# Optimization experiments

Hardware: AMD Instinct MI355X
Metric: run time of the kernel (lower is better)

Reference implementation:

```python
import jax, jax.numpy as jnp
import numpy as np

EMBED = 128; HEADS = 4; NUM_CLASSES = 20; NUM_LAYERS = 2
SCENE = (128, 128, 16)
NQ = SCENE[0] * SCENE[1] * SCENE[2]
NI = 300
IMG = (96, 320); ORI = (384, 1280)
VOXEL_SIZE = 0.2
SCORE_THR, MASK_THR, IOU_THR = 0.25, 0.5, 0.8


def _image_grid():
    # generate_grid(image_shape, ori_image_shape), then flip(dims=[0]) -> (x, y) pixel coords in ori resolution
    ys = jnp.arange(IMG[0], dtype=jnp.float32) * (ORI[0] / IMG[0])
    xs = jnp.arange(IMG[1], dtype=jnp.float32) * (ORI[1] / IMG[1])
    gy, gx = jnp.meshgrid(ys, xs, indexing='ij')
    return jnp.stack([gx, gy], 0)  # (2, h, w)


def _scene_pos():
    g = jnp.stack(jnp.meshgrid(*[jnp.arange(s, dtype=jnp.float32) for s in SCENE], indexing='ij'), 0)
    g = (g + 0.5) * VOXEL_SIZE  # project_scale = 1
    return g.reshape(3, -1).T  # (NQ, 3)


def _layernorm(x, g, b):
    mu = x.mean(-1, keepdims=True)
    var = ((x - mu) ** 2).mean(-1, keepdims=True)
    return (x - mu) * jax.lax.rsqrt(var + 1e-5) * g + b


def _mha(q, k, v, w, b):
    # w: (4, D, D) = Wq, Wk, Wv, Wo; b: (4, D)
    B, Nq, D = q.shape; hd = D // HEADS
    def proj(x, i):
        return (x @ w[i].T + b[i]).reshape(B, -1, HEADS, hd).transpose(0, 2, 1, 3)
    qh, kh, vh = proj(q, 0), proj(k, 1), proj(v, 2)
    attn = jax.nn.softmax(jnp.einsum('bhqd,bhkd->bhqk', qh, kh) / jnp.sqrt(jnp.float32(hd)), axis=-1)
    o = jnp.einsum('bhqk,bhkd->bhqd', attn, vh).transpose(0, 2, 1, 3).reshape(B, Nq, D)
    return o @ w[3].T + b[3]


def _tlayer(q, k, v, aw, ab, lg, lb, w1, b1, w2, b2):
    x = _layernorm(q + _mha(q, k, v, aw, ab), lg[0], lb[0])
    h = jax.nn.relu(x @ w1.T + b1) @ w2.T + b2
    return _layernorm(x + h, lg[1], lb[1])


def setup_inputs():
    key = jax.random.key(0)
    ks = jax.random.split(key, 20)
    h, w = IMG
    queries = jax.random.normal(ks[0], (1, NI, EMBED), jnp.float32)
    # 8 instances get a strong class logit so exactly they pass score_thr
    pred_logits = 0.1 * jax.random.normal(ks[1], (1, NI, NUM_CLASSES + 1), jnp.float32)
    ii = jnp.arange(8)
    pred_logits = pred_logits.at[0, ii, ii % (NUM_CLASSES + 1)].add(6.0)
    # each kept instance owns a disjoint 40-px-wide strip -> passes IoU>=0.8
    pred_masks = -6.0 + 0.1 * jax.random.normal(ks[2], (1, NI, h, w), jnp.float32)
    strip = jnp.arange(w) // 40  # 0..7
    boost = 12.0 * (jnp.arange(NI)[:, None] == strip[None, :]).astype(jnp.float32)
    pred_masks = pred_masks + boost[None, :, None, :]
    x3d = 0.1 * jax.random.normal(ks[3], (1, EMBED) + SCENE, jnp.float32)
    depth = 1.0 + 49.0 * jax.random.uniform(ks[4], (1, h, w), jnp.float32)
    K = jnp.array([[[500.0, 0.0, 160.0], [0.0, 500.0, 48.0], [0.0, 0.0, 1.0]]], jnp.float32)
    E = jnp.array([[[1.0, 0.0, 0.0, 0.5], [0.0, 1.0, 0.0, 1.0], [0.0, 0.0, 1.0, 1.5], [0.0, 0.0, 0.0, 1.0]]], jnp.float32)
    voxel_origin = jnp.array([[[0.0, -12.8, -2.0]]], jnp.float32)
    fov_mask = jax.random.bernoulli(ks[5], 0.25, (1, NQ))
    L = NUM_LAYERS
    scene_embed_w = 0.02 * jax.random.normal(ks[6], (NQ, EMBED), jnp.float32)
    inst_pos_w = 0.02 * jax.random.normal(ks[7], (NI, EMBED), jnp.float32)
    pos_w = 0.02 * jax.random.normal(ks[8], (EMBED, 3), jnp.float32)
    conv_w = 0.05 * jax.random.normal(ks[9], (NUM_CLASSES, EMBED), jnp.float32)
    conv_b = jnp.zeros((NUM_CLASSES,), jnp.float32)
    attn_w = 0.05 * jax.random.normal(ks[10], (L, 2, 4, EMBED, EMBED), jnp.float32)
    attn_b = jnp.zeros((L, 2, 4, EMBED), jnp.float32)
    ln_g = jnp.ones((L, 2, 2, EMBED), jnp.float32)
    ln_b = jnp.zeros((L, 2, 2, EMBED), jnp.float32)
    ffn_w1 = 0.05 * jax.random.normal(ks[11], (L, 2, 4 * EMBED, EMBED), jnp.float32)
    ffn_b1 = jnp.zeros((L, 2, 4 * EMBED), jnp.float32)
    ffn_w2 = 0.05 * jax.random.normal(ks[12], (L, 2, EMBED, 4 * EMBED), jnp.float32)
    ffn_b2 = jnp.zeros((L, 2, EMBED), jnp.float32)
    return dict(queries=queries, pred_logits=pred_logits, pred_masks=pred_masks, x3d=x3d, depth=depth,
                K=K, E=E, voxel_origin=voxel_origin, fov_mask=fov_mask,
                scene_embed_w=scene_embed_w, inst_pos_w=inst_pos_w, pos_w=pos_w, conv_w=conv_w, conv_b=conv_b,
                attn_w=attn_w, attn_b=attn_b, ln_g=ln_g, ln_b=ln_b,
                ffn_w1=ffn_w1, ffn_b1=ffn_b1, ffn_w2=ffn_w2, ffn_b2=ffn_b2)


def reference(queries, pred_logits, pred_masks, x3d, depth, K, E, voxel_origin, fov_mask,
              scene_embed_w, inst_pos_w, pos_w, conv_w, conv_b,
              attn_w, attn_b, ln_g, ln_b, ffn_w1, ffn_b1, ffn_w2, ffn_b2):
    h, w = IMG
    # ---- panoptic_postprocess (bs == 1) ----
    sig = jax.nn.sigmoid(pred_logits[0])
    prob_cls = jax.nn.softmax(sig / 0.06, axis=-1)
    scores = prob_cls.max(-1); labels = prob_cls.argmax(-1)
    keep = (labels != prob_cls.shape[-1]) & (scores > SCORE_THR)
    kidx = jnp.nonzero(keep)[0]
    pm = jax.nn.sigmoid(pred_masks[0])[kidx]          # (k, h, w)
    sk = scores[kidx]
    mids = (sk[:, None, None] * pm).argmax(0)          # per-pixel winning instance
    masks = mids[None] == jnp.arange(pm.shape[0])[:, None, None]
    marea = masks.reshape(pm.shape[0], -1).sum(1)
    pmb = pm >= MASK_THR
    parea = pmb.reshape(pm.shape[0], -1).sum(1)
    masks = masks & pmb
    keep_ = (masks.reshape(pm.shape[0], -1).sum(1) > 0) & (marea / parea >= IOU_THR)
    sel = jnp.nonzero(keep_)[0]
    inst_masks = masks[sel]                             # (k2, h, w)
    k2idx = kidx[sel]                                   # final kept slots in [0, NI)
    # ---- gather_mask_pos (depth already at (h, w) -> interpolate is identity) ----
    ig = _image_grid()
    ig3 = jnp.concatenate([ig[None] * depth[:, None], depth[:, None]], axis=1)  # (1,3,h,w) = (x*d, y*d, d)
    cam = jnp.linalg.inv(K) @ ig3.reshape(1, 3, -1)
    homo = jnp.concatenate([cam, jnp.ones((1, 1, h * w), cam.dtype)], axis=1)
    world = (jnp.linalg.inv(E) @ homo)[0, :3].T        # (hw, 3)
    xyz = inst_masks.reshape(inst_masks.shape[0], -1).astype(world.dtype) @ world  # masked sum per instance
    mask_pos = xyz @ pos_w.T                            # Linear(3, embed, bias=False)
    inst_q = queries[0][k2idx][None]                    # (1, k2, D)
    inst_p = (inst_pos_w[k2idx] + mask_pos)[None]
    # ---- scene tokens ----
    scene_embed_full = scene_embed_w[None] + x3d.reshape(1, EMBED, NQ).transpose(0, 2, 1)
    qsrc = scene_embed_full
    fidx = jnp.nonzero(fov_mask[0])[0]
    se = scene_embed_full[:, fidx]
    sp = ((_scene_pos()[None] + voxel_origin)[:, fidx]) @ pos_w.T
    for i in range(NUM_LAYERS):
        inst_q = _tlayer(inst_q + inst_p, se + sp, se, attn_w[i, 0], attn_b[i, 0], ln_g[i, 0], ln_b[i, 0],
                         ffn_w1[i, 0], ffn_b1[i, 0], ffn_w2[i, 0], ffn_b2[i, 0])
        se = _tlayer(se + sp, inst_q + inst_p, inst_q, attn_w[i, 1], attn_b[i, 1], ln_g[i, 1], ln_b[i, 1],
                     ffn_w1[i, 1], ffn_b1[i, 1], ffn_w2[i, 1], ffn_b2[i, 1])
    # ---- index_fov_back_to_voxels + cls_head (project_scale==1 -> Identity + 1x1 Conv3d) ----
    full = qsrc.at[:, fidx].set(se)
    x3d_ = full.transpose(0, 2, 1).reshape(1, EMBED, *SCENE)
    out = jnp.einsum('bcxyz,oc->boxyz', x3d_, conv_w) + conv_b.reshape(1, -1, 1, 1, 1)
    return out
```

## Files before the change

kernel.cpp:

```cpp
#include <hip/hip_runtime.h>
#include <math.h>

#define EMBED 128
#define NCLS 21
#define NI_ 300
#define IMH 96
#define IMW 320
#define NPIX (IMH*IMW)
#define NQ 262144
#define NF_MAX 73728
#define INST_MAX 16
#define IH_MAX 64
#define RS32 0.17677669529663687f

#define S_NF 0
#define S_NK 1
#define S_NINST 2
#define S_NIH 3
#define S_INVK 8
#define S_INVE 24
#define S_KIDX 64
#define S_SKK 400
#define S_MAREA 768
#define S_PAREA 1088
// ... 173 lines not shown
  int base=blockIdx.x*1024;
  int s=0;
  for (int k=0;k<4;k++) s += (fov[base+k*256+t]!=0)?1:0;
  red[t]=s; __syncthreads();
  for (int st=128;st>0;st>>=1){ if(t<st) red[t]+=red[t+st]; __syncthreads(); }
  if (t==0) iw[S_FCNT+blockIdx.x]=red[0];
}

__global__ void k_fov_scan(float* ws){
  int* iw=(int*)ws;
  if (threadIdx.x==0){
    int acc=0;
    for (int b=0;b<256;b++){ iw[S_FOFF+b]=acc; acc+=iw[S_FCNT+b]; }
    iw[S_NF]=(acc<NF_MAX)?acc:NF_MAX;
  }
}

__global__ __launch_bounds__(256) void k_fov_scatter(const int* fov, float* ws){
  int* iw=(int*)ws;
  int* fidx=(int*)((char*)ws+OFF_FIDX);
  int* invr=(int*)((char*)ws+OFF_INV);
  __shared__ int wsums[4];
  __shared__ int woff[4];
  __shared__ int cur;
  __shared__ int tot;
  int t=threadIdx.x; int w=t>>6; int lane=t&63;
  if (t==0) cur=iw[S_FOFF+blockIdx.x];
  __syncthreads();
  int base=blockIdx.x*1024;
  for (int k=0;k<4;k++){
    int i=base+k*256+t;
    int f=(fov[i]!=0)?1:0;
    unsigned long long m=__ballot(f);
    int rk=__popcll(m & ((lane==0)?0ull:((~0ull)>>(64-lane))));
    if (lane==0) wsums[w]=__popcll(m);
    __syncthreads();
    if (t==0){ int a=0; for(int q2=0;q2<4;q2++){ woff[q2]=a; a+=wsums[q2]; } tot=a; }
    __syncthreads();
    if (f){
      int r=cur+woff[w]+rk;
      if (r<NF_MAX){ fidx[r]=i; invr[i]=r; } else invr[i]=-1;
    } else invr[i]=-1;
    __syncthreads();
    if (t==0) cur+=tot;
    __syncthreads();
  }
}

__global__ __launch_bounds__(256) void k_se_build(const float* sew, const float* x3d, const int* fidx, float* SE, float* ws){
  int* iw=(int*)ws;
  int nf=iw[S_NF];
  int r0=blockIdx.x*64;
  if (r0>=nf) return;
  int nr=min(64,nf-r0);
  __shared__ float tile[64][129];
  __shared__ int fidxl[64];
  int t=threadIdx.x;
  if (t<64) fidxl[t]=(t<nr)? fidx[r0+t]:0;
  __syncthreads();
  for (int idx=t; idx<64*128; idx+=256){
    int v=idx>>7, e=idx&127;
    tile[v][e]=(v<nr)? sew[(size_t)fidxl[v]*128+e]:0.f;
  }
  __syncthreads();
  for (int idx=t; idx<128*64; idx+=256){
    int c=idx>>6, v=idx&63;
    if (v<nr) tile[v][c]+=x3d[(size_t)c*NQ+fidxl[v]];
  }
  __syncthreads();
  for (int idx=t; idx<64*128; idx+=256){
    int v=idx>>7, e=idx&127;
    if (v<nr) SE[(r0+v)*128+e]=tile[v][e];
  }
}

__global__ __launch_bounds__(256) void kA_prep(const float* Wq, const float* bq, const float* Wk, const float* bk, float* ws){
  int* iw=(int*)ws; float* fw=ws;
  int n=iw[S_NINST]; int nih=iw[S_NIH];
  int t=threadIdx.x;
  for (int idx=t; idx<n*128; idx+=256) fw[S_QIN+idx]=fw[S_INSTQ+idx]+fw[S_INSTP+idx];
  __syncthreads();
  for (int idx=t; idx<n*128; idx+=256){
    int i=idx>>7, e=idx&127;
    float a=bq[e];
    for (int k=0;k<128;k++) a+=fw[S_QIN+i*128+k]*Wq[e*128+k];
    fw[S_QH+idx]=a;
  }
  __syncthreads();
  for (int idx=t; idx<nih*128; idx+=256){
    int ih=idx>>7, e=idx&127;
    int i=ih>>2, h=ih&3;
    float a=0.f;
    for (int d=0;d<32;d++) a+=fw[S_QH+i*128+h*32+d]*Wk[(h*32+d)*128+e];
    fw[S_QKT+idx]=a*RS32;
  }
  for (int ih=t; ih<nih; ih+=256){
    int i=ih>>2, h=ih&3;
    float a=0.f;
    for (int d=0;d<32;d++) a+=fw[S_QH+i*128+h*32+d]*bk[h*32+d];
    fw[S_SB+ih]=a*RS32;
  }
}

__global__ __launch_bounds__(256) void kS1(const float* SE, float* SC, const float* posw, const float* org, const int* fidx, float* ws){
  int* iw=(int*)ws; float* fw=ws;
  int nf=iw[S_NF]; int nih=iw[S_NIH];
  int r0=blockIdx.x*64;
  if (r0>=nf || nih==0) return;
  int nr=min(64,nf-r0);
  __shared__ float xt[64][129];
  __shared__ float qk[IH_MAX*128];
  __shared__ float sbl[IH_MAX];
  __shared__ float pwl[384];
  __shared__ float px[64],py[64],pz[64];
  __shared__ int fidxl[64];
  int t=threadIdx.x;
  for (int i=t;i<384;i+=256) pwl[i]=posw[i];
  if (t<64) fidxl[t]=(t<nr)? fidx[r0+t]:0;
  for (int idx=t; idx<nih*128; idx+=256) qk[idx]=fw[S_QKT+idx];
  if (t<IH_MAX) sbl[t]=(t<nih)? fw[S_SB+t]:0.f;
  __syncthreads();
  if (t<64){
    int q=fidxl[t];
    int vx=q>>11, vy=(q>>4)&127, vz=q&15;
    px[t]=(vx+0.5f)*0.2f+org[0];
    py[t]=(vy+0.5f)*0.2f+org[1];
    pz[t]=(vz+0.5f)*0.2f+org[2];
  }
  __syncthreads();
  for (int idx=t; idx<64*128; idx+=256){
    int v=idx>>7, e=idx&127;
    float val=0.f;
    if (v<nr) val=SE[(r0+v)*128+e]+px[v]*pwl[e*3]+py[v]*pwl[e*3+1]+pz[v]*pwl[e*3+2];
    xt[v][e]=val;
  }
  __syncthreads();
  int tokl=t&63, base=t>>6;
  for (int ih=base; ih<nih; ih+=4){
    float a=sbl[ih];
    const float* qrow=qk+ih*128;
    for (int e=0;e<128;e++) a+=qrow[e]*xt[tokl][e];
    if (tokl<nr) SC[(size_t)ih*NF_MAX+r0+tokl]=a;
  }
}

__global__ __launch_bounds__(256) void kS2S3(float* SC, float* ws){
  int* iw=(int*)ws; float* fw=ws;
  int nih=iw[S_NIH]; int ih=blockIdx.x;
  if (ih>=nih) return;
  int nf=iw[S_NF];
  float* row=SC+(size_t)ih*NF_MAX;
  __shared__ float red[256];
  int t=threadIdx.x;
  float m=-1e30f;
  for (int j=t;j<nf;j+=256) m=fmaxf(m,row[j]);
  red[t]=m; __syncthreads();
  for (int s=128;s>0;s>>=1){ if(t<s) red[t]=fmaxf(red[t],red[t+s]); __syncthreads(); }
  m=red[0]; __syncthreads();
  float sum=0.f;
  for (int j=t;j<nf;j+=256){ float p=expf(row[j]-m); row[j]=p; sum+=p; }
  red[t]=sum; __syncthreads();
  for (int s=128;s>0;s>>=1){ if(t<s) red[t]+=red[t+s]; __syncthreads(); }
  if (t==0) fw[S_SUMV+ih]=red[0];
  if (t<128) fw[S_WSUM+ih*128+t]=0.f;
}

__global__ __launch_bounds__(256) void kS4(const float* SC, const float* SE, float* ws){
  int* iw=(int*)ws; float* fw=ws;
  int nf=iw[S_NF]; int nih=iw[S_NIH];
  if (nih==0) return;
  int t=threadIdx.x;
  int chunk=(nf+255)/256;
  int j0=blockIdx.x*chunk;
  int j1=min(nf,j0+chunk);
  if (j0>=j1) return;
  __shared__ float pt[64*64];
  int e=t&127, half=t>>7;
  float acc[32];
  #pragma unroll
  for (int r=0;r<32;r++) acc[r]=0.f;
  for (int jj=j0; jj<j1; jj+=64){
    int cnt=min(64,j1-jj);
    __syncthreads();
    for (int idx=t; idx<64*64; idx+=256){
      int ih=idx>>6, jl=idx&63;
      pt[idx]=(ih<nih && jl<cnt)? SC[(size_t)ih*NF_MAX+jj+jl]:0.f;
    }
    __syncthreads();
    for (int jl=0; jl<cnt; jl++){
      float sv=SE[(jj+jl)*128+e];
      #pragma unroll
      for (int r=0;r<32;r++) acc[r]+=pt[(half*32+r)*64+jl]*sv;
    }
  }
  #pragma unroll
  for (int r=0;r<32;r++) atomicAdd(&fw[S_WSUM+(half*32+r)*128+e], acc[r]);
}

__global__ __launch_bounds__(256) void kA_post(const float* Wv, const float* bv, const float* Wo, const float* bo,
    const float* g, const float* bb, float* ws){
  int* iw=(int*)ws; float* fw=ws;
  int n=iw[S_NINST]; int nih=iw[S_NIH];
  __shared__ float wn[IH_MAX*128];
  __shared__ float ol[INST_MAX*128];
  __shared__ float tl[INST_MAX*128];
  int t=threadIdx.x;
  for (int idx=t; idx<nih*128; idx+=256){
    int ih=idx>>7;
    wn[idx]=fw[S_WSUM+idx]/fw[S_SUMV+ih];
  }
  __syncthreads();
  for (int idx=t; idx<n*128; idx+=256){
    int i=idx>>7, f=idx&127; int h=f>>5;
    float a=bv[f];
    const float* wrow=Wv+f*128;
    const float* wv=wn+(i*4+h)*128;
    for (int e2=0;e2<128;e2++) a+=wrow[e2]*wv[e2];
    ol[idx]=a;
  }
  __syncthreads();
  for (int idx=t; idx<n*128; idx+=256){
    int i=idx>>7, e2=idx&127;
    float a=bo[e2];
    const float* orow=ol+i*128;
    const float* wrow=Wo+e2*128;
    for (int f2=0;f2<128;f2++) a+=orow[f2]*wrow[f2];
    tl[idx]=a+fw[S_QIN+idx];
  }
  __syncthreads();
  int w=t>>6, lane=t&63;
  for (int i=w;i<n;i+=4){
    float v0=tl[i*128+lane], v1=tl[i*128+64+lane];
    float s=v0+v1;
    for (int o=32;o>0;o>>=1) s+=__shfl_xor(s,o);
    float mu=s*(1.f/128.f);
    float d0=v0-mu, d1=v1-mu;
    float vv=d0*d0+d1*d1;
    for (int o=32;o>0;o>>=1) vv+=__shfl_xor(vv,o);
    float rsv=rsqrtf(vv*(1.f/128.f)+1e-5f);
    fw[S_XI+i*128+lane]=d0*rsv*g[lane]+bb[lane];
    fw[S_XI+i*128+64+lane]=d1*rsv*g[64+lane]+bb[64+lane];
  }
}

__global__ __launch_bounds__(256) void kA_ffn(const float* W1, const float* b1, const float* W2, const float* b2,
    const float* g, const float* bb, float* ws){
  int* iw=(int*)ws; float* fw=ws;
  int n=iw[S_NINST];
  int i=blockIdx.x;
  if (i>=n) return;
  __shared__ float xl[128];
  __shared__ float hid[512];
  __shared__ float yv[128];
  int t=threadIdx.x;
  if (t<128) xl[t]=fw[S_XI+i*128+t];
  __syncthreads();
  for (int d=t; d<512; d+=256){
    float a=b1[d];
    const float* wr=W1+d*128;
    for (int k=0;k<128;k++) a+=wr[k]*xl[k];
    hid[d]=fmaxf(a,0.f);
  }
  __syncthreads();
  if (t<128){
    float a=b2[t];
    const float* wr=W2+(size_t)t*512;
    for (int d=0;d<512;d++) a+=wr[d]*hid[d];
    yv[t]=a+xl[t];
  }
  __syncthreads();
  if (t<64){
    float v0=yv[t], v1=yv[t+64];
    float s=v0+v1;
    for (int o=32;o>0;o>>=1) s+=__shfl_xor(s,o);
    float mu=s*(1.f/128.f);
    float d0=v0-mu, d1=v1-mu;
    float vv=d0*d0+d1*d1;
    for (int o=32;o>0;o>>=1) vv+=__shfl_xor(vv,o);
    float rsv=rsqrtf(vv*(1.f/128.f)+1e-5f);
    fw[S_INSTQ+i*128+t]=d0*rsv*g[t]+bb[t];
    fw[S_INSTQ+i*128+64+t]=d1*rsv*g[64+t]+bb[64+t];
  }
}

__global__ __launch_bounds__(256) void kA_kv(const float* Wk2, const float* bk2, const float* Wv2, const float* bv2, float* ws){
  int* iw=(int*)ws; float* fw=ws;
  int n=iw[S_NINST];
  int t=threadIdx.x;
  for (int idx=t; idx<n*128; idx+=256){
    int i=idx>>7, e=idx&127;
    float ak=bk2[e], av=bv2[e];
    const float* wk=Wk2+e*128;
    const float* wv=Wv2+e*128;
    for (int k=0;k<128;k++){
      float qv=fw[S_INSTQ+i*128+k];
      float qp=qv+fw[S_INSTP+i*128+k];
      ak+=qp*wk[k];
      av+=qv*wv[k];
    }
    fw[S_KHB+idx]=ak; fw[S_VHB+idx]=av;
  }
}

__global__ __launch_bounds__(256) void kGEMM(const float* A, float* C, const float* W, const float* bias,
    int mode_in, int mode_out, const float* SE, const int* fidx,
    const float* posw, const float* org, float* ws){
  int* iw=(int*)ws;
  int nf=iw[S_NF];
  int r0=blockIdx.x*64;
  if (r0>=nf) return;
  int c0=blockIdx.y*64;
  __shared__ float As[64][129];
  __shared__ float Wsh[64][129];
  __shared__ float pwl[384];
  __shared__ float px[64],py[64],pz[64];
  int t=threadIdx.x;
  bool needpos=(mode_in==1)||(mode_out==1);
  if (needpos){
    for (int i=t;i<384;i+=256) pwl[i]=posw[i];
    if (t<64){
      int r=r0+t;
      int q=(r<nf)? fidx[r]:0;
      int vx=q>>11, vy=(q>>4)&127, vz=q&15;
      px[t]=(vx+0.5f)*0.2f+org[0];
      py[t]=(vy+0.5f)*0.2f+org[1];
      pz[t]=(vz+0.5f)*0.2f+org[2];
    }
  }
  __syncthreads();
  for (int idx=t; idx<64*128; idx+=256){
    int rl=idx>>7, k=idx&127;
    int r=r0+rl;
    float v=0.f;
    if (r<nf){
      if (mode_in==1) v=SE[r*128+k]+px[rl]*pwl[k*3]+py[rl]*pwl[k*3+1]+pz[rl]*pwl[k*3+2];
      else v=A[r*128+k];
    }
    As[rl][k]=v;
    Wsh[rl][k]=W[(c0+rl)*128+k];
  }
  __syncthreads();
  int tx=t&15, ty=t>>4;
  float acc[4][4];
  #pragma unroll
  for (int i=0;i<4;i++)
    #pragma unroll
    for (int j=0;j<4;j++) acc[i][j]=0.f;
  #pragma unroll 8
  for (int k=0;k<128;k++){
    float a0=As[ty*4+0][k], a1=As[ty*4+1][k], a2=As[ty*4+2][k], a3=As[ty*4+3][k];
    float w0=Wsh[tx*4+0][k], w1=Wsh[tx*4+1][k], w2=Wsh[tx*4+2][k], w3=Wsh[tx*4+3][k];
    acc[0][0]+=a0*w0; acc[0][1]+=a0*w1; acc[0][2]+=a0*w2; acc[0][3]+=a0*w3;
    acc[1][0]+=a1*w0; acc[1][1]+=a1*w1; acc[1][2]+=a1*w2; acc[1][3]+=a1*w3;
    acc[2][0]+=a2*w0; acc[2][1]+=a2*w1; acc[2][2]+=a2*w2; acc[2][3]+=a2*w3;
    acc[3][0]+=a3*w0; acc[3][1]+=a3*w1; acc[3][2]+=a3*w2; acc[3][3]+=a3*w3;
  }
  for (int i=0;i<4;i++){
    int r=r0+ty*4+i;
    if (r>=nf) continue;
    for (int j=0;j<4;j++){
      int c=c0+tx*4+j;
      float v=acc[i][j]+bias[c];
      if (mode_out==1) v+=SE[r*128+c]+px[ty*4+i]*pwl[c*3]+py[ty*4+i]*pwl[c*3+1]+pz[ty*4+i]*pwl[c*3+2];
      C[r*128+c]=v;
    }
  }
}

__global__ __launch_bounds__(256) void kB2(const float* A1, float* A2, float* ws){
  int* iw=(int*)ws; float* fw=ws;
  int nf=iw[S_NF]; int n=iw[S_NINST];
  int r0=blockIdx.x*64;
  if (r0>=nf) return;
  __shared__ float kh[INST_MAX*128];
  __shared__ float vh[INST_MAX*128];
  __shared__ float ot[64][129];
  int t=threadIdx.x;
  for (int idx=t; idx<INST_MAX*128; idx+=256){
    kh[idx]=(idx<n*128)? fw[S_KHB+idx]:0.f;
    vh[idx]=(idx<n*128)? fw[S_VHB+idx]:0.f;
  }
  __syncthreads();
  int tokl=t&63, h=t>>6;
  int r=r0+tokl;
  bool valid=r<nf;
  float q[32];
  #pragma unroll
  for (int d=0;d<32;d++) q[d]=valid? A1[r*128+h*32+d]:0.f;
  float s[INST_MAX]; float mx=-1e30f;
  for (int j=0;j<INST_MAX;j++){
    float a=0.f;
    #pragma unroll
    for (int d=0;d<32;d++) a+=q[d]*kh[j*128+h*32+d];
    a*=RS32;
    s[j]=(j<n)? a:-1e30f;
    mx=fmaxf(mx,s[j]);
  }
  float sum=0.f;
  for (int j=0;j<INST_MAX;j++){ float p=expf(s[j]-mx); s[j]=p; sum+=p; }
  float inv=(n>0)? 1.0f/sum:0.f;
  float o[32];
  #pragma unroll
  for (int d=0;d<32;d++) o[d]=0.f;
  for (int j=0;j<INST_MAX;j++){
    float a=s[j]*inv;
    #pragma unroll
    for (int d=0;d<32;d++) o[d]+=a*vh[j*128+h*32+d];
  }
  #pragma unroll
  for (int d=0;d<32;d++) ot[tokl][h*32+d]=o[d];
  __syncthreads();
  for (int idx=t; idx<64*128; idx+=256){
    int rl=idx>>7, e=idx&127;
    if (r0+rl<nf) A2[(r0+rl)*128+e]=ot[rl][e];
  }
}

__global__ __launch_bounds__(256) void kLN(const float* A, float* B, const float* g, const float* b, float* ws){
  int* iw=(int*)ws;
  int nf=iw[S_NF];
  int t=threadIdx.x; int w=t>>6; int lane=t&63;
  int r=blockIdx.x*4+w;
  if (r>=nf) return;
  float v0=A[r*128+lane], v1=A[r*128+64+lane];
  float s=v0+v1;
  for (int o=32;o>0;o>>=1) s+=__shfl_xor(s,o);
  float mu=s*(1.0f/128.0f);
  float d0=v0-mu, d1=v1-mu;
  float vv=d0*d0+d1*d1;
  for (int o=32;o>0;o>>=1) vv+=__shfl_xor(vv,o);
  float rsv=rsqrtf(vv*(1.0f/128.0f)+1e-5f);
  B[r*128+lane]=d0*rsv*g[lane]+b[lane];
  B[r*128+64+lane]=d1*rsv*g[64+lane]+b[64+lane];
}

__global__ void k_transpose(const float* in, float* outp, int R, int C){
  __shared__ float tile[32][33];
  int bx=blockIdx.x*32, by=blockIdx.y*32;
  int tx=threadIdx.x, ty=threadIdx.y;
  for (int k=0;k<4;k++){
    int r=by+ty+k*8, c=bx+tx;
    if (r<R && c<C) tile[ty+k*8][tx]=in[(size_t)r*C+c];
  }
  __syncthreads();
  for (int k=0;k<4;k++){
    int cc=bx+ty+k*8, rr=by+tx;
    if (rr<R && cc<C) outp[(size_t)cc*R+rr]=tile[tx][ty+k*8];
  }
}

__global__ __launch_bounds__(256) void kFFN(const float* X_, float* SEo, const float* W1T, const float* W2T,
    const float* b1, const float* b2, const float* g, const float* bb, float* ws){
  int* iw=(int*)ws;
  int nf=iw[S_NF];
  int r0=blockIdx.x*64;
  if (r0>=nf) return;
  __shared__ float Xs[64][132];
  __shared__ float Hs[64][68];
  int t=threadIdx.x;
  int tx=t&15, ty=t>>4;
  int ty4=ty*4;
  int ecol=tx*8;
  for (int idx=t; idx<64*32; idx+=256){
    int rl=idx>>5, e4=idx&31;
    int r=r0+rl;
    float4 v = (r<nf)? reinterpret_cast<const float4*>(X_+(size_t)r*128)[e4]
                     : make_float4(0.f,0.f,0.f,0.f);
    *reinterpret_cast<float4*>(&Xs[rl][e4*4]) = v;
  }
  __syncthreads();
  float yacc[4][8];
  #pragma unroll
  for (int i=0;i<4;i++)
    #pragma unroll
    for (int j=0;j<8;j++) yacc[i][j]=0.f;
  for (int dc=0; dc<512; dc+=64){
    int dcol = dc + tx*4;
    float acc[4][4];
    #pragma unroll
    for (int i=0;i<4;i++)
      #pragma unroll
      for (int j=0;j<4;j++) acc[i][j]=0.f;
    for (int k=0;k<128;k+=4){
      float4 w0=*reinterpret_cast<const float4*>(W1T+(size_t)(k+0)*512+dcol);
      float4 w1=*reinterpret_cast<const float4*>(W1T+(size_t)(k+1)*512+dcol);
      float4 w2=*reinterpret_cast<const float4*>(W1T+(size_t)(k+2)*512+dcol);
      float4 w3=*reinterpret_cast<const float4*>(W1T+(size_t)(k+3)*512+dcol);
      #pragma unroll
      for (int i=0;i<4;i++){
        float4 xv=*reinterpret_cast<const float4*>(&Xs[ty4+i][k]);
        acc[i][0]+=xv.x*w0.x; acc[i][1]+=xv.x*w0.y; acc[i][2]+=xv.x*w0.z; acc[i][3]+=xv.x*w0.w;
        acc[i][0]+=xv.y*w1.x; acc[i][1]+=xv.y*w1.y; acc[i][2]+=xv.y*w1.z; acc[i][3]+=xv.y*w1.w;
        acc[i][0]+=xv.z*w2.x; acc[i][1]+=xv.z*w2.y; acc[i][2]+=xv.z*w2.z; acc[i][3]+=xv.z*w2.w;
        acc[i][0]+=xv.w*w3.x; acc[i][1]+=xv.w*w3.y; acc[i][2]+=xv.w*w3.z; acc[i][3]+=xv.w*w3.w;
      }
    }
    float4 b1v=*reinterpret_cast<const float4*>(b1+dcol);
    #pragma unroll
    for (int i=0;i<4;i++){
      float4 h;
      h.x=fmaxf(acc[i][0]+b1v.x,0.f);
      h.y=fmaxf(acc[i][1]+b1v.y,0.f);
      h.z=fmaxf(acc[i][2]+b1v.z,0.f);
      h.w=fmaxf(acc[i][3]+b1v.w,0.f);
      *reinterpret_cast<float4*>(&Hs[ty4+i][tx*4])=h;
    }
    __syncthreads();
    for (int d=0; d<64; d+=4){
      float4 ha0=*reinterpret_cast<const float4*>(&Hs[ty4+0][d]);
      float4 ha1=*reinterpret_cast<const float4*>(&Hs[ty4+1][d]);
      float4 ha2=*reinterpret_cast<const float4*>(&Hs[ty4+2][d]);
      float4 ha3=*reinterpret_cast<const float4*>(&Hs[ty4+3][d]);
      #pragma unroll
      for (int kk=0;kk<4;kk++){
        const float* wrow=W2T+(size_t)(dc+d+kk)*128+ecol;
        float4 wa=*reinterpret_cast<const float4*>(wrow);
        float4 wb=*reinterpret_cast<const float4*>(wrow+4);
        float h0 = (kk==0)?ha0.x:(kk==1)?ha0.y:(kk==2)?ha0.z:ha0.w;
        float h1 = (kk==0)?ha1.x:(kk==1)?ha1.y:(kk==2)?ha1.z:ha1.w;
        float h2 = (kk==0)?ha2.x:(kk==1)?ha2.y:(kk==2)?ha2.z:ha2.w;
        float h3 = (kk==0)?ha3.x:(kk==1)?ha3.y:(kk==2)?ha3.z:ha3.w;
        yacc[0][0]+=h0*wa.x; yacc[0][1]+=h0*wa.y; yacc[0][2]+=h0*wa.z; yacc[0][3]+=h0*wa.w;
        yacc[0][4]+=h0*wb.x; yacc[0][5]+=h0*wb.y; yacc[0][6]+=h0*wb.z; yacc[0][7]+=h0*wb.w;
        yacc[1][0]+=h1*wa.x; yacc[1][1]+=h1*wa.y; yacc[1][2]+=h1*wa.z; yacc[1][3]+=h1*wa.w;
        yacc[1][4]+=h1*wb.x; yacc[1][5]+=h1*wb.y; yacc[1][6]+=h1*wb.z; yacc[1][7]+=h1*wb.w;
        yacc[2][0]+=h2*wa.x; yacc[2][1]+=h2*wa.y; yacc[2][2]+=h2*wa.z; yacc[2][3]+=h2*wa.w;
        yacc[2][4]+=h2*wb.x; yacc[2][5]+=h2*wb.y; yacc[2][6]+=h2*wb.z; yacc[2][7]+=h2*wb.w;
        yacc[3][0]+=h3*wa.x; yacc[3][1]+=h3*wa.y; yacc[3][2]+=h3*wa.z; yacc[3][3]+=h3*wa.w;
        yacc[3][4]+=h3*wb.x; yacc[3][5]+=h3*wb.y; yacc[3][6]+=h3*wb.z; yacc[3][7]+=h3*wb.w;
      }
    }
    __syncthreads();
  }
  float4 b2a=*reinterpret_cast<const float4*>(b2+ecol);
  float4 b2b=*reinterpret_cast<const float4*>(b2+ecol+4);
  #pragma unroll
  for (int i=0;i<4;i++){
    float4 xa=*reinterpret_cast<const float4*>(&Xs[ty4+i][ecol]);
    float4 xb=*reinterpret_cast<const float4*>(&Xs[ty4+i][ecol+4]);
    xa.x+=yacc[i][0]+b2a.x; xa.y+=yacc[i][1]+b2a.y; xa.z+=yacc[i][2]+b2a.z; xa.w+=yacc[i][3]+b2a.w;
    xb.x+=yacc[i][4]+b2b.x; xb.y+=yacc[i][5]+b2b.y; xb.z+=yacc[i][6]+b2b.z; xb.w+=yacc[i][7]+b2b.w;
    *reinterpret_cast<float4*>(&Xs[ty4+i][ecol])=xa;
    *reinterpret_cast<float4*>(&Xs[ty4+i][ecol+4])=xb;
  }
  __syncthreads();
  int w=t>>6, lane=t&63;
  for (int rl=w; rl<64; rl+=4){
    int r=r0+rl;
    float v0=Xs[rl][lane], v1=Xs[rl][64+lane];
    float s=v0+v1;
    for (int o=32;o>0;o>>=1) s+=__shfl_xor(s,o);
    float mu=s*(1.f/128.f);
    float d0=v0-mu, d1=v1-mu;
    float vv=d0*d0+d1*d1;
    for (int o=32;o>0;o>>=1) vv+=__shfl_xor(vv,o);
    float rsv=rsqrtf(vv*(1.f/128.f)+1e-5f);
    if (r<nf){
      SEo[r*128+lane]=d0*rsv*g[lane]+bb[lane];
      SEo[r*128+64+lane]=d1*rsv*g[64+lane]+bb[64+lane];
    }
  }
}

__global__ __launch_bounds__(256) void k_out(const float* SE, const float* sew, const float* x3d,
    const float* convw, const float* convb, const int* invr, float* out, float* ws){
  (void)ws;
  __shared__ float rows[64][129];
  __shared__ float cw[20*128];
  __shared__ float cb[20];
  __shared__ int rkl[64];
  int t=threadIdx.x;
  int q0=blockIdx.x*64;
  for (int idx=t; idx<20*128; idx+=256) cw[idx]=convw[idx];
  if (t<20) cb[t]=convb[t];
  if (t<64) rkl[t]=invr[q0+t];
  __syncthreads();
  for (int idx=t; idx<64*128; idx+=256){
    int v=idx>>7, e=idx&127;
    int rk=rkl[v];
    rows[v][e]=(rk>=0)? SE[rk*128+e]:sew[(size_t)(q0+v)*128+e];
  }
  __syncthreads();
  for (int idx=t; idx<128*64; idx+=256){
    int c=idx>>6, v=idx&63;
    if (rkl[v]<0) rows[v][c]+=x3d[(size_t)c*NQ+q0+v];
  }
  __syncthreads();
  int v=t&63;
  for (int o=t>>6; o<20; o+=4){
    float a=cb[o];
    const float* cr=cw+o*128;
    for (int c=0;c<128;c++) a+=rows[v][c]*cr[c];
    out[(size_t)o*NQ+q0+v]=a;
  }
}

extern "C" void kernel_launch(void* const* d_in, const int* in_sizes, int n_in,
                              void* d_out, int out_size, void* d_ws, size_t ws_size,
                              hipStream_t stream){
  (void)in_sizes; (void)n_in; (void)out_size; (void)ws_size;
  const float* queries  = (const float*)d_in[0];
  const float* plogits  = (const float*)d_in[1];
  const float* pmasks   = (const float*)d_in[2];
  const float* x3d      = (const float*)d_in[3];
  const float* depth    = (const float*)d_in[4];
  const float* Kmat     = (const float*)d_in[5];
  const float* Emat     = (const float*)d_in[6];
  const float* vorigin  = (const float*)d_in[7];
  const int*   fov      = (const int*)d_in[8];
  const float* sew      = (const float*)d_in[9];
  const float* instposw = (const float*)d_in[10];
  const float* posw     = (const float*)d_in[11];
  const float* convw    = (const float*)d_in[12];
  const float* convb    = (const float*)d_in[13];
  const float* AW       = (const float*)d_in[14];
  const float* AB       = (const float*)d_in[15];
  const float* LG       = (const float*)d_in[16];
  const float* LB       = (const float*)d_in[17];
  const float* F1W      = (const float*)d_in[18];
  const float* F1B      = (const float*)d_in[19];
  const float* F2W      = (const float*)d_in[20];
  const float* F2B      = (const float*)d_in[21];
  float* out = (float*)d_out;
  char* wsb = (char*)d_ws;
  float* fws = (float*)d_ws;
  int* fidx = (int*)(wsb + OFF_FIDX);
  int* invr = (int*)(wsb + OFF_INV);
  float* W1T = (float*)(wsb + OFF_W1T);
  float* W2T = (float*)(wsb + OFF_W2T);
  float* SE = (float*)(wsb + OFF_SE);
  float* A1 = (float*)(wsb + OFF_A1);
  float* A2 = (float*)(wsb + OFF_A2);
  float* SC = (float*)(wsb + OFF_SC);

  auto aw  = [&](int i,int br,int m){ return AW + (size_t)(((i*2+br)*4+m))*128*128; };
  auto ab  = [&](int i,int br,int m){ return AB + (size_t)(((i*2+br)*4+m))*128; };
  auto lng = [&](int i,int br,int wch){ return LG + (size_t)(((i*2+br)*2+wch))*128; };
  auto lnb = [&](int i,int br,int wch){ return LB + (size_t)(((i*2+br)*2+wch))*128; };
  auto f1w = [&](int i,int br){ return F1W + (size_t)(i*2+br)*512*128; };
  auto f1b = [&](int i,int br){ return F1B + (size_t)(i*2+br)*512; };
  auto f2w = [&](int i,int br){ return F2W + (size_t)(i*2+br)*128*512; };
  auto f2b = [&](int i,int br){ return F2B + (size_t)(i*2+br)*128; };

  const int NB64 = NF_MAX/64;
  const int NB4  = NF_MAX/4;

  k_init<<<1,256,0,stream>>>(Kmat,Emat,fws);
  k_score<<<1,320,0,stream>>>(plogits,fws);
  k_winner<<<NPIX/256,256,0,stream>>>(pmasks,depth,fws);
  k_sel<<<1,256,0,stream>>>(queries,instposw,posw,fws);
  k_fov_count<<<256,256,0,stream>>>(fov,fws);
  k_fov_scan<<<1,64,0,stream>>>(fws);
  k_fov_scatter<<<256,256,0,stream>>>(fov,fws);
  k_se_build<<<NB64,256,0,stream>>>(sew,x3d,fidx,SE,fws);

  for (int i=0;i<2;i++){
    kA_prep<<<1,256,0,stream>>>(aw(i,0,0),ab(i,0,0),aw(i,0,1),ab(i,0,1),fws);
    kS1<<<NB64,256,0,stream>>>(SE,SC,posw,vorigin,fidx,fws);
    kS2S3<<<IH_MAX,256,0,stream>>>(SC,fws);
    kS4<<<256,256,0,stream>>>(SC,SE,fws);
    kA_post<<<1,256,0,stream>>>(aw(i,0,2),ab(i,0,2),aw(i,0,3),ab(i,0,3),lng(i,0,0),lnb(i,0,0),fws);
    kA_ffn<<<INST_MAX,256,0,stream>>>(f1w(i,0),f1b(i,0),f2w(i,0),f2b(i,0),lng(i,0,1),lnb(i,0,1),fws);
    kA_kv<<<1,256,0,stream>>>(aw(i,1,1),ab(i,1,1),aw(i,1,2),ab(i,1,2),fws);
    kGEMM<<<dim3(NB64,2),256,0,stream>>>(nullptr,A1,aw(i,1,0),ab(i,1,0),1,0,SE,fidx,posw,vorigin,fws);
    kB2<<<NB64,256,0,stream>>>(A1,A2,fws);
    kGEMM<<<dim3(NB64,2),256,0,stream>>>(A2,A1,aw(i,1,3),ab(i,1,3),0,1,SE,fidx,posw,vorigin,fws);
    kLN<<<NB4,256,0,stream>>>(A1,A2,lng(i,1,0),lnb(i,1,0),fws);
    k_transpose<<<dim3(4,16),dim3(32,8),0,stream>>>(f1w(i,1),W1T,512,128);
    k_transpose<<<dim3(16,4),dim3(32,8),0,stream>>>(f2w(i,1),W2T,128,512);
    kFFN<<<NB64,256,0,stream>>>(A2,SE,W1T,W2T,f1b(i,1),f2b(i,1),lng(i,1,1),lnb(i,1,1),fws);
  }
  k_out<<<NQ/64,256,0,stream>>>(SE,sew,x3d,convw,convb,invr,out,fws);
}
```

Measured before the change: 2.580 ms.

## Fuse scene-branch attention, output projection and layernorm into one kernel

Replaces the generic two-launch Q GEMM, attention, output GEMM and layernorm sequence with two kernels. kQ computes the full 128-column Q projection per 64-row block with float4 loads, reading weights directly from global memory. kAttnOLN does attention, the Wo projection, the residual and positional add, and the layernorm in registers and shared memory. This removes intermediate global round-trips and launches, at the cost of reading weights uncached from global memory in the inner loop and higher register pressure.

```diff
diff --git a/kernel.cpp b/kernel.cpp
--- a/kernel.cpp
+++ b/kernel.cpp
@@ -499,136 +499,213 @@
   }
 }
 
-__global__ __launch_bounds__(256) void kGEMM(const float* A, float* C, const float* W, const float* bias,
-    int mode_in, int mode_out, const float* SE, const int* fidx,
-    const float* posw, const float* org, float* ws){
+__global__ __launch_bounds__(256) void kQ(float* __restrict__ A1,
+    const float* __restrict__ Wq, const float* __restrict__ bq,
+    const float* __restrict__ SE, const int* __restrict__ fidx,
+    const float* __restrict__ posw, const float* __restrict__ org, float* __restrict__ ws){
   int* iw=(int*)ws;
   int nf=iw[S_NF];
   int r0=blockIdx.x*64;
   if (r0>=nf) return;
-  int c0=blockIdx.y*64;
-  __shared__ float As[64][129];
-  __shared__ float Wsh[64][129];
+  __shared__ float Xs[64][132];
   __shared__ float pwl[384];
   __shared__ float px[64],py[64],pz[64];
   int t=threadIdx.x;
-  bool needpos=(mode_in==1)||(mode_out==1);
-  if (needpos){
-    for (int i=t;i<384;i+=256) pwl[i]=posw[i];
-    if (t<64){
-      int r=r0+t;
-      int q=(r<nf)? fidx[r]:0;
-      int vx=q>>11, vy=(q>>4)&127, vz=q&15;
-      px[t]=(vx+0.5f)*0.2f+org[0];
-      py[t]=(vy+0.5f)*0.2f+org[1];
-      pz[t]=(vz+0.5f)*0.2f+org[2];
-    }
-  }
-  __syncthreads();
-  for (int idx=t; idx<64*128; idx+=256){
-    int rl=idx>>7, k=idx&127;
-    int r=r0+rl;
-    float v=0.f;
-    if (r<nf){
-      if (mode_in==1) v=SE[r*128+k]+px[rl]*pwl[k*3]+py[rl]*pwl[k*3+1]+pz[rl]*pwl[k*3+2];
-      else v=A[r*128+k];
-    }
-    As[rl][k]=v;
-    Wsh[rl][k]=W[(c0+rl)*128+k];
-  }
-  __syncthreads();
-  int tx=t&15, ty=t>>4;
-  float acc[4][4];
+  for (int i=t;i<384;i+=256) pwl[i]=posw[i];
+  if (t<64){
+    int r=r0+t;
+    int q=(r<nf)? fidx[r]:0;
+    int vx=q>>11, vy=(q>>4)&127, vz=q&15;
+    px[t]=(vx+0.5f)*0.2f+org[0];
+    py[t]=(vy+0.5f)*0.2f+org[1];
+    pz[t]=(vz+0.5f)*0.2f+org[2];
+  }
+  __syncthreads();
+  for (int idx=t; idx<64*32; idx+=256){
+    int rl=idx>>5, e4=(idx&31)*4;
+    float4 v=*reinterpret_cast<const float4*>(SE+(size_t)(r0+rl)*128+e4);
+    float X=px[rl], Y=py[rl], Z=pz[rl];
+    v.x+=X*pwl[(e4+0)*3]+Y*pwl[(e4+0)*3+1]+Z*pwl[(e4+0)*3+2];
+    v.y+=X*pwl[(e4+1)*3]+Y*pwl[(e4+1)*3+1]+Z*pwl[(e4+1)*3+2];
+    v.z+=X*pwl[(e4+2)*3]+Y*pwl[(e4+2)*3+1]+Z*pwl[(e4+2)*3+2];
+    v.w+=X*pwl[(e4+3)*3]+Y*pwl[(e4+3)*3+1]+Z*pwl[(e4+3)*3+2];
+    *reinterpret_cast<float4*>(&Xs[rl][e4])=v;
+  }
+  __syncthreads();
+  int tx=t&15, ty=t>>4, ty4=ty*4, ecol=tx*8;
+  float acc[4][8];
   #pragma unroll
   for (int i=0;i<4;i++)
     #pragma unroll
-    for (int j=0;j<4;j++) acc[i][j]=0.f;
-  #pragma unroll 8
-  for (int k=0;k<128;k++){
-    float a0=As[ty*4+0][k], a1=As[ty*4+1][k], a2=As[ty*4+2][k], a3=As[ty*4+3][k];
-    float w0=Wsh[tx*4+0][k], w1=Wsh[tx*4+1][k], w2=Wsh[tx*4+2][k], w3=Wsh[tx*4+3][k];
-    acc[0][0]+=a0*w0; acc[0][1]+=a0*w1; acc[0][2]+=a0*w2; acc[0][3]+=a0*w3;
-    acc[1][0]+=a1*w0; acc[1][1]+=a1*w1; acc[1][2]+=a1*w2; acc[1][3]+=a1*w3;
-    acc[2][0]+=a2*w0; acc[2][1]+=a2*w1; acc[2][2]+=a2*w2; acc[2][3]+=a2*w3;
-    acc[3][0]+=a3*w0; acc[3][1]+=a3*w1; acc[3][2]+=a3*w2; acc[3][3]+=a3*w3;
-  }
+    for (int j=0;j<8;j++) acc[i][j]=0.f;
+  for (int k=0;k<128;k+=4){
+    float4 xv0=*reinterpret_cast<const float4*>(&Xs[ty4+0][k]);
+    float4 xv1=*reinterpret_cast<const float4*>(&Xs[ty4+1][k]);
+    float4 xv2=*reinterpret_cast<const float4*>(&Xs[ty4+2][k]);
+    float4 xv3=*reinterpret_cast<const float4*>(&Xs[ty4+3][k]);
+    #pragma unroll
+    for (int jj=0;jj<8;jj++){
+      float4 w=*reinterpret_cast<const float4*>(Wq+(size_t)(ecol+jj)*128+k);
+      acc[0][jj]+=xv0.x*w.x+xv0.y*w.y+xv0.z*w.z+xv0.w*w.w;
+      acc[1][jj]+=xv1.x*w.x+xv1.y*w.y+xv1.z*w.z+xv1.w*w.w;
+      acc[2][jj]+=xv2.x*w.x+xv2.y*w.y+xv2.z*w.z+xv2.w*w.w;
+      acc[3][jj]+=xv3.x*w.x+xv3.y*w.y+xv3.z*w.z+xv3.w*w.w;
+    }
+  }
+  float4 bqa=*reinterpret_cast<const float4*>(bq+ecol);
+  float4 bqb=*reinterpret_cast<const float4*>(bq+ecol+4);
+  #pragma unroll
   for (int i=0;i<4;i++){
-    int r=r0+ty*4+i;
+    int r=r0+ty4+i;
     if (r>=nf) continue;
-    for (int j=0;j<4;j++){
-      int c=c0+tx*4+j;
-      float v=acc[i][j]+bias[c];
-      if (mode_out==1) v+=SE[r*128+c]+px[ty*4+i]*pwl[c*3]+py[ty*4+i]*pwl[c*3+1]+pz[ty*4+i]*pwl[c*3+2];
-      C[r*128+c]=v;
-    }
-  }
-}
-
-__global__ __launch_bounds__(256) void kB2(const float* A1, float* A2, float* ws){
+    float4 o1, o2;
+    o1.x=acc[i][0]+bqa.x; o1.y=acc[i][1]+bqa.y; o1.z=acc[i][2]+bqa.z; o1.w=acc[i][3]+bqa.w;
+    o2.x=acc[i][4]+bqb.x; o2.y=acc[i][5]+bqb.y; o2.z=acc[i][6]+bqb.z; o2.w=acc[i][7]+bqb.w;
+    *reinterpret_cast<float4*>(A1+(size_t)r*128+ecol)=o1;
+    *reinterpret_cast<float4*>(A1+(size_t)r*128+ecol+4)=o2;
+  }
+}
+
+__global__ __launch_bounds__(256) void kAttnOLN(const float* __restrict__ A1, float* __restrict__ A2,
+    const float* __restrict__ Wo, const float* __restrict__ bo,
+    const float* __restrict__ g, const float* __restrict__ bb,
+    const float* __restrict__ SE, const int* __restrict__ fidx,
+    const float* __restrict__ posw, const float* __restrict__ org, float* __restrict__ ws){
   int* iw=(int*)ws; float* fw=ws;
   int nf=iw[S_NF]; int n=iw[S_NINST];
   int r0=blockIdx.x*64;
   if (r0>=nf) return;
+  __shared__ float ot[64][132];
   __shared__ float kh[INST_MAX*128];
   __shared__ float vh[INST_MAX*128];
-  __shared__ float ot[64][129];
+  __shared__ float pwl[384];
+  __shared__ float px[64],py[64],pz[64];
   int t=threadIdx.x;
   for (int idx=t; idx<INST_MAX*128; idx+=256){
     kh[idx]=(idx<n*128)? fw[S_KHB+idx]:0.f;
     vh[idx]=(idx<n*128)? fw[S_VHB+idx]:0.f;
   }
-  __syncthreads();
-  int tokl=t&63, h=t>>6;
-  int r=r0+tokl;
-  bool valid=r<nf;
-  float q[32];
+  for (int i=t;i<384;i+=256) pwl[i]=posw[i];
+  if (t<64){
+    int r=r0+t;
+    int q=(r<nf)? fidx[r]:0;
+    int vx=q>>11, vy=(q>>4)&127, vz=q&15;
+    px[t]=(vx+0.5f)*0.2f+org[0];
+    py[t]=(vy+0.5f)*0.2f+org[1];
+    pz[t]=(vz+0.5f)*0.2f+org[2];
+  }
+  for (int idx=t; idx<64*32; idx+=256){
+    int rl=idx>>5, e4=(idx&31)*4;
+    *reinterpret_cast<float4*>(&ot[rl][e4]) =
+      *reinterpret_cast<const float4*>(A1+(size_t)(r0+rl)*128+e4);
+  }
+  __syncthreads();
+  {
+    int tokl=t&63, h=t>>6;
+    float q[32];
+    #pragma unroll
+    for (int d8=0;d8<8;d8++){
+      float4 v=*reinterpret_cast<const float4*>(&ot[tokl][h*32+d8*4]);
+      q[d8*4]=v.x; q[d8*4+1]=v.y; q[d8*4+2]=v.z; q[d8*4+3]=v.w;
+    }
+    float s[INST_MAX]; float mx=-1e30f;
+    for (int j=0;j<INST_MAX;j++){
+      float a=0.f;
+      #pragma unroll
+      for (int d4=0;d4<8;d4++){
+        float4 kv=*reinterpret_cast<const float4*>(&kh[j*128+h*32+d4*4]);
+        a+=q[d4*4]*kv.x+q[d4*4+1]*kv.y+q[d4*4+2]*kv.z+q[d4*4+3]*kv.w;
+      }
+      a*=RS32;
+      s[j]=(j<n)? a:-1e30f;
+      mx=fmaxf(mx,s[j]);
+    }
+    float sum=0.f;
+    for (int j=0;j<INST_MAX;j++){ float p=expf(s[j]-mx); s[j]=p; sum+=p; }
+    float inv=(n>0)? 1.0f/sum:0.f;
+    float o[32];
+    #pragma unroll
+    for (int d=0;d<32;d++) o[d]=0.f;
+    for (int j=0;j<INST_MAX;j++){
+      float a=s[j]*inv;
+      #pragma unroll
+      for (int d4=0;d4<8;d4++){
+        float4 vv=*reinterpret_cast<const float4*>(&vh[j*128+h*32+d4*4]);
+        o[d4*4]+=a*vv.x; o[d4*4+1]+=a*vv.y; o[d4*4+2]+=a*vv.z; o[d4*4+3]+=a*vv.w;
+      }
+    }
+    #pragma unroll
+    for (int d8=0;d8<8;d8++){
+      float4 v; v.x=o[d8*4]; v.y=o[d8*4+1]; v.z=o[d8*4+2]; v.w=o[d8*4+3];
+      *reinterpret_cast<float4*>(&ot[tokl][h*32+d8*4])=v;
+    }
+  }
+  __syncthreads();
+  int tx=t&15, ty=t>>4, ty4=ty*4, ecol=tx*8;
+  float acc[4][8];
   #pragma unroll
-  for (int d=0;d<32;d++) q[d]=valid? A1[r*128+h*32+d]:0.f;
-  float s[INST_MAX]; float mx=-1e30f;
-  for (int j=0;j<INST_MAX;j++){
-    float a=0.f;
-    #pragma unroll
-    for (int d=0;d<32;d++) a+=q[d]*kh[j*128+h*32+d];
-    a*=RS32;
-    s[j]=(j<n)? a:-1e30f;
-    mx=fmaxf(mx,s[j]);
-  }
-  float sum=0.f;
-  for (int j=0;j<INST_MAX;j++){ float p=expf(s[j]-mx); s[j]=p; sum+=p; }
-  float inv=(n>0)? 1.0f/sum:0.f;
-  float o[32];
+  for (int i=0;i<4;i++)
+    #pragma unroll
+    for (int j=0;j<8;j++) acc[i][j]=0.f;
+  for (int k=0;k<128;k+=4){
+    float4 xv0=*reinterpret_cast<const float4*>(&ot[ty4+0][k]);
+    float4 xv1=*reinterpret_cast<const float4*>(&ot[ty4+1][k]);
+    float4 xv2=*reinterpret_cast<const float4*>(&ot[ty4+2][k]);
+    float4 xv3=*reinterpret_cast<const float4*>(&ot[ty4+3][k]);
+    #pragma unroll
+    for (int jj=0;jj<8;jj++){
+      float4 w=*reinterpret_cast<const float4*>(Wo+(size_t)(ecol+jj)*128+k);
+      acc[0][jj]+=xv0.x*w.x+xv0.y*w.y+xv0.z*w.z+xv0.w*w.w;
+      acc[1][jj]+=xv1.x*w.x+xv1.y*w.y+xv1.z*w.z+xv1.w*w.w;
+      acc[2][jj]+=xv2.x*w.x+xv2.y*w.y+xv2.z*w.z+xv2.w*w.w;
+      acc[3][jj]+=xv3.x*w.x+xv3.y*w.y+xv3.z*w.z+xv3.w*w.w;
+    }
+  }
+  float4 boa=*reinterpret_cast<const float4*>(bo+ecol);
+  float4 bob=*reinterpret_cast<const float4*>(bo+ecol+4);
+  float4 ga=*reinterpret_cast<const float4*>(g+ecol);
+  float4 gb=*reinterpret_cast<const float4*>(g+ecol+4);
+  float4 ba=*reinterpret_cast<const float4*>(bb+ecol);
+  float4 bbv=*reinterpret_cast<const float4*>(bb+ecol+4);
+  float pe[8][3];
   #pragma unroll
-  for (int d=0;d<32;d++) o[d]=0.f;
-  for (int j=0;j<INST_MAX;j++){
-    float a=s[j]*inv;
-    #pragma unroll
-    for (int d=0;d<32;d++) o[d]+=a*vh[j*128+h*32+d];
+  for (int jj=0;jj<8;jj++){
+    pe[jj][0]=pwl[(ecol+jj)*3]; pe[jj][1]=pwl[(ecol+jj)*3+1]; pe[jj][2]=pwl[(ecol+jj)*3+2];
   }
   #pragma unroll
-  for (int d=0;d<32;d++) ot[tokl][h*32+d]=o[d];
-  __syncthreads();
-  for (int idx=t; idx<64*128; idx+=256){
-    int rl=idx>>7, e=idx&127;
-    if (r0+rl<nf) A2[(r0+rl)*128+e]=ot[rl][e];
-  }
-}
-
-__global__ __launch_bounds__(256) void kLN(const float* A, float* B, const float* g, const float* b, float* ws){
-  int* iw=(int*)ws;
-  int nf=iw[S_NF];
-  int t=threadIdx.x; int w=t>>6; int lane=t&63;
-  int r=blockIdx.x*4+w;
-  if (r>=nf) return;
-  float v0=A[r*128+lane], v1=A[r*128+64+lane];
-  float s=v0+v1;
-  for (int o=32;o>0;o>>=1) s+=__shfl_xor(s,o);
-  float mu=s*(1.0f/128.0f);
-  float d0=v0-mu, d1=v1-mu;
-  float vv=d0*d0+d1*d1;
-  for (int o=32;o>0;o>>=1) vv+=__shfl_xor(vv,o);
-  float rsv=rsqrtf(vv*(1.0f/128.0f)+1e-5f);
-  B[r*128+lane]=d0*rsv*g[lane]+b[lane];
-  B[r*128+64+lane]=d1*rsv*g[64+lane]+b[64+lane];
+  for (int i=0;i<4;i++){
+    int r=r0+ty4+i;
+    float4 se1=*reinterpret_cast<const float4*>(SE+(size_t)r*128+ecol);
+    float4 se2=*reinterpret_cast<const float4*>(SE+(size_t)r*128+ecol+4);
+    float X=px[ty4+i], Y=py[ty4+i], Z=pz[ty4+i];
+    acc[i][0]+=boa.x+se1.x+X*pe[0][0]+Y*pe[0][1]+Z*pe[0][2];
+    acc[i][1]+=boa.y+se1.y+X*pe[1][0]+Y*pe[1][1]+Z*pe[1][2];
+    acc[i][2]+=boa.z+se1.z+X*pe[2][0]+Y*pe[2][1]+Z*pe[2][2];
+    acc[i][3]+=boa.w+se1.w+X*pe[3][0]+Y*pe[3][1]+Z*pe[3][2];
+    acc[i][4]+=bob.x+se2.x+X*pe[4][0]+Y*pe[4][1]+Z*pe[4][2];
+    acc[i][5]+=bob.y+se2.y+X*pe[5][0]+Y*pe[5][1]+Z*pe[5][2];
+    acc[i][6]+=bob.z+se2.z+X*pe[6][0]+Y*pe[6][1]+Z*pe[6][2];
+    acc[i][7]+=bob.w+se2.w+X*pe[7][0]+Y*pe[7][1]+Z*pe[7][2];
+    float s1=0.f;
+    #pragma unroll
+    for (int jj=0;jj<8;jj++) s1+=acc[i][jj];
+    s1+=__shfl_xor(s1,1); s1+=__shfl_xor(s1,2); s1+=__shfl_xor(s1,4); s1+=__shfl_xor(s1,8);
+    float mu=s1*(1.f/128.f);
+    float vv=0.f;
+    #pragma unroll
+    for (int jj=0;jj<8;jj++){ float d=acc[i][jj]-mu; acc[i][jj]=d; vv+=d*d; }
+    vv+=__shfl_xor(vv,1); vv+=__shfl_xor(vv,2); vv+=__shfl_xor(vv,4); vv+=__shfl_xor(vv,8);
+    float rsv=rsqrtf(vv*(1.f/128.f)+1e-5f);
+    if (r<nf){
+      float4 o1,o2;
+      o1.x=acc[i][0]*rsv*ga.x+ba.x; o1.y=acc[i][1]*rsv*ga.y+ba.y;
+      o1.z=acc[i][2]*rsv*ga.z+ba.z; o1.w=acc[i][3]*rsv*ga.w+ba.w;
+      o2.x=acc[i][4]*rsv*gb.x+bbv.x; o2.y=acc[i][5]*rsv*gb.y+bbv.y;
+      o2.z=acc[i][6]*rsv*gb.z+bbv.z; o2.w=acc[i][7]*rsv*gb.w+bbv.w;
+      *reinterpret_cast<float4*>(A2+(size_t)r*128+ecol)=o1;
+      *reinterpret_cast<float4*>(A2+(size_t)r*128+ecol+4)=o2;
+    }
+  }
 }
 
 __global__ void k_transpose(const float* in, float* outp, int R, int C){
@@ -840,7 +917,6 @@
   auto f2b = [&](int i,int br){ return F2B + (size_t)(i*2+br)*128; };
 
   const int NB64 = NF_MAX/64;
-  const int NB4  = NF_MAX/4;
 
   k_init<<<1,256,0,stream>>>(Kmat,Emat,fws);
   k_score<<<1,320,0,stream>>>(plogits,fws);
@@ -859,10 +935,8 @@
     kA_post<<<1,256,0,stream>>>(aw(i,0,2),ab(i,0,2),aw(i,0,3),ab(i,0,3),lng(i,0,0),lnb(i,0,0),fws);
     kA_ffn<<<INST_MAX,256,0,stream>>>(f1w(i,0),f1b(i,0),f2w(i,0),f2b(i,0),lng(i,0,1),lnb(i,0,1),fws);
     kA_kv<<<1,256,0,stream>>>(aw(i,1,1),ab(i,1,1),aw(i,1,2),ab(i,1,2),fws);
-    kGEMM<<<dim3(NB64,2),256,0,stream>>>(nullptr,A1,aw(i,1,0),ab(i,1,0),1,0,SE,fidx,posw,vorigin,fws);
-    kB2<<<NB64,256,0,stream>>>(A1,A2,fws);
-    kGEMM<<<dim3(NB64,2),256,0,stream>>>(A2,A1,aw(i,1,3),ab(i,1,3),0,1,SE,fidx,posw,vorigin,fws);
-    kLN<<<NB4,256,0,stream>>>(A1,A2,lng(i,1,0),lnb(i,1,0),fws);
+    kQ<<<NB64,256,0,stream>>>(A1,aw(i,1,0),ab(i,1,0),SE,fidx,posw,vorigin,fws);
+    kAttnOLN<<<NB64,256,0,stream>>>(A1,A2,aw(i,1,3),ab(i,1,3),lng(i,1,0),lnb(i,1,0),SE,fidx,posw,vorigin,fws);
     k_transpose<<<dim3(4,16),dim3(32,8),0,stream>>>(f1w(i,1),W1T,512,128);
     k_transpose<<<dim3(16,4),dim3(32,8),0,stream>>>(f2w(i,1),W2T,128,512);
     kFFN<<<NB64,256,0,stream>>>(A2,SE,W1T,W2T,f1b(i,1),f2b(i,1),lng(i,1,1),lnb(i,1,1),fws);
```

Measured after the change: 2.607 ms. About the same (+1.0%).
